# Kernel optimization log

Measured on AMD Instinct MI355X. Metric: run time of the kernel, lower is better.

The kernel has to match this reference:

```python
import jax, jax.numpy as jnp
import numpy as np

HIDDEN = 1024
N_HEADS = 16
N_KV = 4
HEAD_DIM = HIDDEN // N_HEADS  # 64


def setup_inputs() -> dict:
    key = jax.random.key(0)
    ks = jax.random.split(key, 10)
    B, S, D = 2, 2048, HIDDEN
    s = 0.02
    return {
        "hidden_states": jax.random.normal(ks[0], (B, S, D), jnp.float32),
        "attention_mask": jnp.ones((B, S), jnp.float32),
        "Wq": jax.random.normal(ks[1], (D, N_HEADS * HEAD_DIM), jnp.float32) * s,
        "bq": jnp.zeros((N_HEADS * HEAD_DIM,), jnp.float32),
        "Wk": jax.random.normal(ks[2], (D, N_KV * HEAD_DIM), jnp.float32) * s,
        "bk": jnp.zeros((N_KV * HEAD_DIM,), jnp.float32),
        "Wv": jax.random.normal(ks[3], (D, N_KV * HEAD_DIM), jnp.float32) * s,
        "bv": jnp.zeros((N_KV * HEAD_DIM,), jnp.float32),
        "Wo": jax.random.normal(ks[4], (D, D), jnp.float32) * s,
        "bo": jnp.zeros((D,), jnp.float32),
    }


def _rope(x):
    # x: [B, H, S, Dh]; half-split RoPE as in the torch module
    S, Dh = x.shape[-2], x.shape[-1]
    inv_freq = 1.0 / (10000.0 ** (jnp.arange(0, Dh, 2, dtype=jnp.float32) / Dh))
    freqs = jnp.arange(S, dtype=jnp.float32)[:, None] * inv_freq[None, :]  # [S, Dh/2]
    cos, sin = jnp.cos(freqs), jnp.sin(freqs)
    x1, x2 = jnp.split(x, 2, axis=-1)
    return jnp.concatenate([x1 * cos - x2 * sin, x1 * sin + x2 * cos], axis=-1)


def reference(hidden_states, attention_mask, Wq, bq, Wk, bk, Wv, bv, Wo, bo):
    B, S, D = hidden_states.shape
    q = (hidden_states @ Wq + bq).reshape(B, S, N_HEADS, HEAD_DIM).transpose(0, 2, 1, 3)
    k = (hidden_states @ Wk + bk).reshape(B, S, N_KV, HEAD_DIM).transpose(0, 2, 1, 3)
    v = (hidden_states @ Wv + bv).reshape(B, S, N_KV, HEAD_DIM).transpose(0, 2, 1, 3)
    q = _rope(q)
    k = _rope(k)
    rep = N_HEADS // N_KV
    k = jnp.repeat(k, rep, axis=1)  # [B, H, S, Dh]
    v = jnp.repeat(v, rep, axis=1)
    bias = (1.0 - attention_mask[:, None, None, :]) * -1e9  # [B,1,1,S]
    scores = jnp.einsum("bhqd,bhkd->bhqk", q, k) / jnp.sqrt(jnp.float32(HEAD_DIM))
    attn = jax.nn.softmax(scores + bias, axis=-1)
    out = jnp.einsum("bhqk,bhkd->bhqd", attn, v)
    out = out.transpose(0, 2, 1, 3).reshape(B, S, D)
    return out @ Wo + bo
```

## Files before the change

kernel.cpp:

```cpp
#include <hip/hip_runtime.h>

typedef __bf16 bf16;
typedef __attribute__((ext_vector_type(8))) __bf16 bf16x8;
typedef __attribute__((ext_vector_type(4))) __bf16 bf16x4;
typedef __attribute__((ext_vector_type(4))) float f32x4;

#define LOG2E 1.44269504088896340736f
#define QSCALE 0.18033688011112042f

__device__ inline void tr_tile(const float* __restrict__ in, bf16* __restrict__ out,
                               int R, int C, int bx, int by, int tid) {
    __shared__ float t[32][33];
    int tx = tid & 31, ty = tid >> 5;
    int rbase = by * 32, cbase = bx * 32;
#pragma unroll
    for (int i = 0; i < 4; i++) {
        int r = ty + i * 8;
        t[r][tx] = in[(size_t)(rbase + r) * C + cbase + tx];
    }
    __syncthreads();
#pragma unroll
    for (int i = 0; i < 4; i++) {
        int r = ty + i * 8;
        out[(size_t)(cbase + r) * R + rbase + tx] = (bf16)t[tx][r];
    }
}

__global__ __launch_bounds__(256) void prep_k(const float* __restrict__ X,
                                              const float* __restrict__ Wq,
                                              const float* __restrict__ Wk,
                                              const float* __restrict__ Wv,
                                              const float* __restrict__ Wo,
                                              const float* __restrict__ mask,
                                              bf16* __restrict__ Xb,
                                              bf16* __restrict__ WqT,
                                              bf16* __restrict__ WkT,
                                              bf16* __restrict__ WvT,
                                              bf16* __restrict__ WoT,
                                              float2* __restrict__ rt,
                                              float* __restrict__ Mb,
                                              int* __restrict__ mflags) {
    int blk = blockIdx.x, tid = threadIdx.x;
    if (blk < 2048) {
        int idx = (blk * 256 + tid) * 8;
        float4 a = *(const float4*)(X + idx);
        float4 b = *(const float4*)(X + idx + 4);
        bf16 v[8] = {(bf16)a.x, (bf16)a.y, (bf16)a.z, (bf16)a.w,
                     (bf16)b.x, (bf16)b.y, (bf16)b.z, (bf16)b.w};
        *(uint4*)(Xb + idx) = *(const uint4*)v;
    } else if (blk < 3072) {
        int t = blk - 2048; tr_tile(Wq, WqT, 1024, 1024, t & 31, t >> 5, tid);
    } else if (blk < 3328) {
        int t = blk - 3072; tr_tile(Wk, WkT, 1024, 256, t & 7, t >> 3, tid);
    } else if (blk < 3584) {
        int t = blk - 3328; tr_tile(Wv, WvT, 1024, 256, t & 7, t >> 3, tid);
    } else if (blk < 4608) {
        int t = blk - 3584; tr_tile(Wo, WoT, 1024, 1024, t & 31, t >> 5, tid);
    } else if (blk < 4864) {
        int idx = (blk - 4608) * 256 + tid;
        int s = idx >> 5, i = idx & 31;
        float inv = exp2f(-0.41524100370589830f * (float)i);
        float ang = (float)s * inv;
        rt[idx] = make_float2(cosf(ang), sinf(ang));
    } else {
        __shared__ int sflag;
        int b = blk - 4864;
        if (tid == 0) sflag = 1;
        __syncthreads();
        const float* mrow = mask + (size_t)b * 2048;
        int i0 = tid * 8;
        bool ones = true;
#pragma unroll
        for (int j = 0; j < 8; j++) {
            float m = mrow[i0 + j];
            if (m != 1.0f) ones = false;
            Mb[(size_t)b * 2048 + i0 + j] = (1.0f - m) * (-1e9f) * LOG2E;
        }
        if (!ones) sflag = 0;
        __syncthreads();
        if (tid == 0) mflags[b] = sflag;
    }
}

__global__ __launch_bounds__(256) void vtrans_k(const unsigned short* __restrict__ in,
                                                unsigned short* __restrict__ out) {
    __shared__ unsigned short t[32][33];
    int z = blockIdx.z;
    const unsigned short* ip = in + (size_t)z * 2048 * 64;
    unsigned short* op = out + (size_t)z * 2048 * 64;
    int tx = threadIdx.x & 31, ty = threadIdx.x >> 5;
    int rbase = blockIdx.y * 32, cbase = blockIdx.x * 32;
#pragma unroll
    for (int i = 0; i < 4; i++) {
        int r = ty + i * 8;
        t[r][tx] = ip[(size_t)(rbase + r) * 64 + cbase + tx];
    }
    __syncthreads();
#pragma unroll
    for (int i = 0; i < 4; i++) {
        int r = ty + i * 8;
        op[(size_t)(cbase + r) * 2048 + rbase + tx] = t[tx][r];
    }
}

__device__ __forceinline__ void gemm_main_12864(const bf16* __restrict__ A,
                                                const bf16* __restrict__ BT,
                                                int m0, int n0, int tid,
                                                f32x4 (&acc)[2][4]) {
    __shared__ bf16 As[128 * 64];
    __shared__ bf16 Bs[64 * 64];
    int w = tid >> 6, lane = tid & 63, l15 = lane & 15, quad = lane >> 4;

    int srow = lane >> 3;
    int kx = ((lane & 7) ^ srow) * 8;
    const bf16* ga0 = A + (size_t)(m0 + w * 32 + srow) * 1024 + kx;
    const bf16* gb0 = BT + (size_t)(n0 + w * 16 + srow) * 1024 + kx;
    bf16* la0 = As + (w * 32) * 64 + lane * 8;
    bf16* lb0 = Bs + (w * 16) * 64 + lane * 8;

    for (int k0 = 0; k0 < 1024; k0 += 64) {
#pragma unroll
        for (int p = 0; p < 4; p++)
            __builtin_amdgcn_global_load_lds(
                (const __attribute__((address_space(1))) unsigned int*)(ga0 + (size_t)p * 8 * 1024 + k0),
                (__attribute__((address_space(3))) unsigned int*)(la0 + p * 512), 16, 0, 0);
#pragma unroll
        for (int p = 0; p < 2; p++)
            __builtin_amdgcn_global_load_lds(
                (const __attribute__((address_space(1))) unsigned int*)(gb0 + (size_t)p * 8 * 1024 + k0),
                (__attribute__((address_space(3))) unsigned int*)(lb0 + p * 512), 16, 0, 0);
        __syncthreads();
#pragma unroll
        for (int half = 0; half < 2; half++) {
            bf16x8 a[2], bfr[4];
            int kp = ((half * 4 + quad) ^ (l15 & 7)) * 8;
#pragma unroll
            for (int i = 0; i < 2; i++)
                a[i] = *(const bf16x8*)&As[(w * 32 + i * 16 + l15) * 64 + kp];
#pragma unroll
            for (int j = 0; j < 4; j++)
                bfr[j] = *(const bf16x8*)&Bs[(j * 16 + l15) * 64 + kp];
#pragma unroll
            for (int i = 0; i < 2; i++)
#pragma unroll
                for (int j = 0; j < 4; j++)
                    acc[i][j] = __builtin_amdgcn_mfma_f32_16x16x32_bf16(a[i], bfr[j], acc[i][j], 0, 0, 0);
        }
        __syncthreads();
    }
}

__global__ __launch_bounds__(256) void qkv_gemm2(const bf16* __restrict__ Xb,
                                                 const bf16* __restrict__ WTall,
                                                 const float* __restrict__ bq,
                                                 const float* __restrict__ bk,
                                                 const float* __restrict__ bv,
                                                 const float2* __restrict__ rt,
                                                 bf16* __restrict__ Qb,
                                                 bf16* __restrict__ Kb,
                                                 bf16* __restrict__ Vb) {
    int tt = blockIdx.x, gy = blockIdx.y, tid = threadIdx.x;
    f32x4 acc[2][4] = {};
    gemm_main_12864(Xb, WTall, tt * 128, gy * 64, tid, acc);

    int w = tid >> 6, lane = tid & 63, l15 = lane & 15, quad = lane >> 4;
    const float* bias;
    bf16* dst;
    int mode, head;
    if (gy < 16)      { head = gy;      bias = bq + head * 64; dst = Qb; mode = 0; }
    else if (gy < 20) { head = gy - 16; bias = bk + head * 64; dst = Kb; mode = 1; }
    else              { head = gy - 20; bias = bv + head * 64; dst = Vb; mode = 2; }

#pragma unroll
    for (int i = 0; i < 2; i++) {
#pragma unroll
        for (int r = 0; r < 4; r++) {
            int token = tt * 128 + w * 32 + i * 16 + quad * 4 + r;
            int b = token >> 11, s = token & 2047;
            float vals[4];
#pragma unroll
            for (int j = 0; j < 4; j++) vals[j] = acc[i][j][r] + bias[j * 16 + l15];
            if (mode <= 1) {
#pragma unroll
                for (int c = 0; c < 2; c++) {
                    float2 cs2 = rt[s * 32 + c * 16 + l15];
                    float x1 = vals[c], x2 = vals[c + 2];
                    vals[c]     = x1 * cs2.x - x2 * cs2.y;
                    vals[c + 2] = x1 * cs2.y + x2 * cs2.x;
                }
            }
            if (mode == 0) {
#pragma unroll
                for (int j = 0; j < 4; j++) vals[j] *= QSCALE;
            }
            size_t base;
            if (mode == 0) base = (((size_t)b * 16 + head) * 2048 + s) * 64;
            else           base = (((size_t)b * 4  + head) * 2048 + s) * 64;
#pragma unroll
            for (int j = 0; j < 4; j++) dst[base + j * 16 + l15] = (bf16)vals[j];
        }
    }
}

__global__ __launch_bounds__(256) void oproj_gemm2(const bf16* __restrict__ Ab,
                                                   const bf16* __restrict__ WoT,
                                                   const float* __restrict__ bo,
                                                   float* __restrict__ out) {
    int tt = blockIdx.x, nt = blockIdx.y, tid = threadIdx.x;
    f32x4 acc[2][4] = {};
    gemm_main_12864(Ab, WoT, tt * 128, nt * 64, tid, acc);

    int w = tid >> 6, lane = tid & 63, l15 = lane & 15, quad = lane >> 4;
#pragma unroll
    for (int i = 0; i < 2; i++) {
#pragma unroll
        for (int r = 0; r < 4; r++) {
            int token = tt * 128 + w * 32 + i * 16 + quad * 4 + r;
#pragma unroll
            for (int j = 0; j < 4; j++) {
                int n = nt * 64 + j * 16 + l15;
                out[(size_t)token * 1024 + n] = acc[i][j][r] + bo[n];
            }
        }
    }
}

__global__ __launch_bounds__(256) void attn_k(const bf16* __restrict__ Qb,
                                              const bf16* __restrict__ Kb,
                                              const bf16* __restrict__ VbT,
                                              const float* __restrict__ Mb,
                                              const int* __restrict__ mflags,
                                              bf16* __restrict__ Ob) {
    int qt = blockIdx.x, h = blockIdx.y, b = blockIdx.z;
    int kvh = h >> 2;

    __shared__ bf16 Ks[2][64 * 64];
    __shared__ bf16 Vs[2][64 * 64];
    __shared__ unsigned short Ps[4][32 * 72];

    int tid = threadIdx.x, w = tid >> 6, lane = tid & 63, l15 = lane & 15, quad = lane >> 4;

    const bool maskOnes = (mflags[b] != 0);

    bf16x8 qa[2][2];
#pragma unroll
    for (int g = 0; g < 2; g++) {
        size_t qbase = (((size_t)b * 16 + h) * 2048 + (size_t)qt * 128 + w * 32 + g * 16 + l15) * 64;
        qa[g][0] = *(const bf16x8*)(Qb + qbase + quad * 8);
        qa[g][1] = *(const bf16x8*)(Qb + qbase + 32 + quad * 8);
    }

    f32x4 oacc[2][4] = {};
    float lsum[2] = {0.f, 0.f};

    size_t kRow = ((size_t)b * 4 + kvh) * 2048;
    size_t vRow = ((size_t)b * 4 + kvh) * 64;
    const float* mrow = Mb + (size_t)b * 2048 + quad * 4;

    int srow = (lane >> 3);
    int kx = ((lane & 7) ^ srow) * 8;
    const bf16* gk0 = Kb + (kRow + w * 16 + srow) * 64 + kx;
    const bf16* gv0 = VbT + (vRow + w * 16 + srow) * 2048 + kx;
    int lofs = (w * 16) * 64 + lane * 8;

#define STAGE(KT, BUF)                                                                              \
    do {                                                                                            \
        _Pragma("unroll")                                                                           \
        for (int p = 0; p < 2; p++) {                                                               \
            __builtin_amdgcn_global_load_lds(                                                       \
                (const __attribute__((address_space(1))) unsigned int*)(gk0 + ((size_t)(KT) * 64 + p * 8) * 64), \
                (__attribute__((address_space(3))) unsigned int*)(&Ks[BUF][0] + lofs + p * 512), 16, 0, 0); \
            __builtin_amdgcn_global_load_lds(                                                       \
                (const __attribute__((address_space(1))) unsigned int*)(gv0 + (size_t)p * 8 * 2048 + (KT) * 64), \
                (__attribute__((address_space(3))) unsigned int*)(&Vs[BUF][0] + lofs + p * 512), 16, 0, 0); \
        }                                                                                           \
    } while (0)

    STAGE(0, 0);
    __syncthreads();

    for (int kt = 0; kt < 32; kt++) {
        int cb = kt & 1;
        if (kt < 31) STAGE(kt + 1, cb ^ 1);

        const bf16* ksb = &Ks[cb][0];
        const bf16* vsb = &Vs[cb][0];

        bf16x8 ka[4][2];
#pragma unroll
        for (int c = 0; c < 4; c++) {
            int row = c * 16 + l15;
#pragma unroll
            for (int half = 0; half < 2; half++) {
                int kp = ((half * 4 + quad) ^ (l15 & 7)) * 8;
                ka[c][half] = *(const bf16x8*)&ksb[row * 64 + kp];
            }
        }

        f32x4 sc[2][4];
#pragma unroll
        for (int g = 0; g < 2; g++)
#pragma unroll
            for (int c = 0; c < 4; c++) {
                f32x4 z = {};
                z = __builtin_amdgcn_mfma_f32_16x16x32_bf16(ka[c][0], qa[g][0], z, 0, 0, 0);
                z = __builtin_amdgcn_mfma_f32_16x16x32_bf16(ka[c][1], qa[g][1], z, 0, 0, 0);
                sc[g][c] = z;
            }
        if (!maskOnes) {
#pragma unroll
            for (int c = 0; c < 4; c++) {
                f32x4 bias4 = *(const f32x4*)(mrow + kt * 64 + c * 16);
#pragma unroll
                for (int r = 0; r < 4; r++) { sc[0][c][r] += bias4[r]; sc[1][c][r] += bias4[r]; }
            }
        }

#pragma unroll
        for (int g = 0; g < 2; g++) {
            float rs = 0.f;
#pragma unroll
            for (int c = 0; c < 4; c++)
#pragma unroll
                for (int r = 0; r < 4; r++) { sc[g][c][r] = exp2f(sc[g][c][r]); rs += sc[g][c][r]; }
            lsum[g] += rs;
#pragma unroll
            for (int c = 0; c < 4; c++) {
                bf16x4 pv = {(bf16)sc[g][c][0], (bf16)sc[g][c][1], (bf16)sc[g][c][2], (bf16)sc[g][c][3]};
                *(bf16x4*)&Ps[w][(g * 16 + l15) * 72 + c * 16 + quad * 4] = pv;
            }
        }

        bf16x8 vb[4][2];
#pragma unroll
        for (int c = 0; c < 4; c++) {
            int row = c * 16 + l15;
#pragma unroll
            for (int half = 0; half < 2; half++) {
                int kp = ((half * 4 + quad) ^ (l15 & 7)) * 8;
                vb[c][half] = *(const bf16x8*)&vsb[row * 64 + kp];
            }
        }
        bf16x8 pa[2][2];
#pragma unroll
        for (int g = 0; g < 2; g++) {
            pa[g][0] = *(const bf16x8*)&Ps[w][(g * 16 + l15) * 72 + quad * 8];
            pa[g][1] = *(const bf16x8*)&Ps[w][(g * 16 + l15) * 72 + 32 + quad * 8];
        }
#pragma unroll
        for (int g = 0; g < 2; g++)
#pragma unroll
            for (int c = 0; c < 4; c++) {
                oacc[g][c] = __builtin_amdgcn_mfma_f32_16x16x32_bf16(pa[g][0], vb[c][0], oacc[g][c], 0, 0, 0);
                oacc[g][c] = __builtin_amdgcn_mfma_f32_16x16x32_bf16(pa[g][1], vb[c][1], oacc[g][c], 0, 0, 0);
            }
        __syncthreads();
    }
#undef STAGE

#pragma unroll
    for (int g = 0; g < 2; g++) {
        lsum[g] += __shfl_xor(lsum[g], 16, 64);
        lsum[g] += __shfl_xor(lsum[g], 32, 64);
        float linv[4];
#pragma unroll
        for (int r = 0; r < 4; r++) linv[r] = 1.0f / __shfl(lsum[g], quad * 4 + r, 64);
#pragma unroll
        for (int r = 0; r < 4; r++) {
            int q = qt * 128 + w * 32 + g * 16 + quad * 4 + r;
            size_t base = ((size_t)b * 2048 + q) * 1024 + h * 64;
#pragma unroll
            for (int c = 0; c < 4; c++) Ob[base + c * 16 + l15] = (bf16)(oacc[g][c][r] * linv[r]);
        }
    }
}

extern "C" void kernel_launch(void* const* d_in, const int* in_sizes, int n_in,
                              void* d_out, int out_size, void* d_ws, size_t ws_size,
                              hipStream_t stream) {
    const float* X    = (const float*)d_in[0];
    const float* mask = (const float*)d_in[1];
    const float* Wq   = (const float*)d_in[2];
    const float* bq   = (const float*)d_in[3];
    const float* Wk   = (const float*)d_in[4];
    const float* bk   = (const float*)d_in[5];
    const float* Wv   = (const float*)d_in[6];
    const float* bv   = (const float*)d_in[7];
    const float* Wo   = (const float*)d_in[8];
    const float* bo   = (const float*)d_in[9];
    float* out = (float*)d_out;
    bf16* ws  = (bf16*)d_ws;

    bf16* Xb  = ws;
    bf16* WqT = Xb + (size_t)4096 * 1024;
    bf16* WkT = WqT + 1024 * 1024;
    bf16* WvT = WkT + 256 * 1024;
    bf16* WoT = WvT + 256 * 1024;
    bf16* Qb  = WoT + 1024 * 1024;
    bf16* Kb  = Qb + (size_t)2 * 16 * 2048 * 64;
    bf16* Vb  = Kb + (size_t)2 * 4 * 2048 * 64;
    bf16* Ab  = Vb + (size_t)2 * 4 * 2048 * 64;
    float2* rt = (float2*)(Ab + (size_t)2 * 2048 * 1024);
    float* Mb  = (float*)(rt + 2048 * 32);
    int* mflags = (int*)(Mb + 2 * 2048);
    bf16* VbT = Xb;

    prep_k<<<4866, 256, 0, stream>>>(X, Wq, Wk, Wv, Wo, mask, Xb, WqT, WkT, WvT, WoT, rt, Mb, mflags);
    qkv_gemm2<<<dim3(32, 24), 256, 0, stream>>>(Xb, WqT, bq, bk, bv, rt, Qb, Kb, Vb);
    vtrans_k<<<dim3(2, 64, 8), 256, 0, stream>>>((const unsigned short*)Vb, (unsigned short*)VbT);
    attn_k<<<dim3(16, 16, 2), 256, 0, stream>>>(Qb, Kb, VbT, Mb, mflags, Ab);
    oproj_gemm2<<<dim3(32, 16), 256, 0, stream>>>(Ab, WoT, bo, out);
}
```

Before: 196.5 us.

## Write V transposed from QKV GEMM and feed P from registers into MFMA

The QKV GEMM epilogue now writes V directly in transposed [d][s] layout, so the separate vtrans kernel launch and its extra global round trip go away. In the attention kernel, the softmax probabilities stay in registers as bf16x4 fragments and feed 16x16x16 MFMAs directly, removing the per-wave shared-memory P buffer and its store/load traffic. The costs are strided 2-byte global stores for V in the GEMM epilogue, and twice as many smaller MFMA instructions in the PV product.

```diff
diff --git a/kernel.cpp b/kernel.cpp
--- a/kernel.cpp
+++ b/kernel.cpp
@@ -4,9 +4,21 @@
 typedef __attribute__((ext_vector_type(8))) __bf16 bf16x8;
 typedef __attribute__((ext_vector_type(4))) __bf16 bf16x4;
 typedef __attribute__((ext_vector_type(4))) float f32x4;
+typedef __attribute__((ext_vector_type(4))) short short4v;
 
 #define LOG2E 1.44269504088896340736f
 #define QSCALE 0.18033688011112042f
+
+static __device__ __forceinline__ f32x4 mfma16x16x16bf16(bf16x4 a, bf16x4 b, f32x4 c) {
+#if __has_builtin(__builtin_amdgcn_mfma_f32_16x16x16_bf16)
+    return __builtin_amdgcn_mfma_f32_16x16x16_bf16(a, b, c, 0, 0, 0);
+#else
+    short4v as, bs;
+    __builtin_memcpy(&as, &a, 8);
+    __builtin_memcpy(&bs, &b, 8);
+    return __builtin_amdgcn_mfma_f32_16x16x16bf16_1k(as, bs, c, 0, 0, 0);
+#endif
+}
 
 __device__ inline void tr_tile(const float* __restrict__ in, bf16* __restrict__ out,
                                int R, int C, int bx, int by, int tid) {
@@ -82,27 +94,6 @@
     }
 }
 
-__global__ __launch_bounds__(256) void vtrans_k(const unsigned short* __restrict__ in,
-                                                unsigned short* __restrict__ out) {
-    __shared__ unsigned short t[32][33];
-    int z = blockIdx.z;
-    const unsigned short* ip = in + (size_t)z * 2048 * 64;
-    unsigned short* op = out + (size_t)z * 2048 * 64;
-    int tx = threadIdx.x & 31, ty = threadIdx.x >> 5;
-    int rbase = blockIdx.y * 32, cbase = blockIdx.x * 32;
-#pragma unroll
-    for (int i = 0; i < 4; i++) {
-        int r = ty + i * 8;
-        t[r][tx] = ip[(size_t)(rbase + r) * 64 + cbase + tx];
-    }
-    __syncthreads();
-#pragma unroll
-    for (int i = 0; i < 4; i++) {
-        int r = ty + i * 8;
-        op[(size_t)(cbase + r) * 2048 + rbase + tx] = t[tx][r];
-    }
-}
-
 __device__ __forceinline__ void gemm_main_12864(const bf16* __restrict__ A,
                                                 const bf16* __restrict__ BT,
                                                 int m0, int n0, int tid,
@@ -158,18 +149,17 @@
                                                  const float2* __restrict__ rt,
                                                  bf16* __restrict__ Qb,
                                                  bf16* __restrict__ Kb,
-                                                 bf16* __restrict__ Vb) {
+                                                 bf16* __restrict__ VbT) {
     int tt = blockIdx.x, gy = blockIdx.y, tid = threadIdx.x;
     f32x4 acc[2][4] = {};
     gemm_main_12864(Xb, WTall, tt * 128, gy * 64, tid, acc);
 
     int w = tid >> 6, lane = tid & 63, l15 = lane & 15, quad = lane >> 4;
     const float* bias;
-    bf16* dst;
     int mode, head;
-    if (gy < 16)      { head = gy;      bias = bq + head * 64; dst = Qb; mode = 0; }
-    else if (gy < 20) { head = gy - 16; bias = bk + head * 64; dst = Kb; mode = 1; }
-    else              { head = gy - 20; bias = bv + head * 64; dst = Vb; mode = 2; }
+    if (gy < 16)      { head = gy;      bias = bq + head * 64; mode = 0; }
+    else if (gy < 20) { head = gy - 16; bias = bk + head * 64; mode = 1; }
+    else              { head = gy - 20; bias = bv + head * 64; mode = 2; }
 
 #pragma unroll
     for (int i = 0; i < 2; i++) {
@@ -192,12 +182,18 @@
             if (mode == 0) {
 #pragma unroll
                 for (int j = 0; j < 4; j++) vals[j] *= QSCALE;
-            }
-            size_t base;
-            if (mode == 0) base = (((size_t)b * 16 + head) * 2048 + s) * 64;
-            else           base = (((size_t)b * 4  + head) * 2048 + s) * 64;
-#pragma unroll
-            for (int j = 0; j < 4; j++) dst[base + j * 16 + l15] = (bf16)vals[j];
+                size_t base = (((size_t)b * 16 + head) * 2048 + s) * 64;
+#pragma unroll
+                for (int j = 0; j < 4; j++) Qb[base + j * 16 + l15] = (bf16)vals[j];
+            } else if (mode == 1) {
+                size_t base = (((size_t)b * 4 + head) * 2048 + s) * 64;
+#pragma unroll
+                for (int j = 0; j < 4; j++) Kb[base + j * 16 + l15] = (bf16)vals[j];
+            } else {
+                size_t vbase = ((size_t)b * 4 + head) * 64 * 2048 + s;
+#pragma unroll
+                for (int j = 0; j < 4; j++) VbT[vbase + (size_t)(j * 16 + l15) * 2048] = (bf16)vals[j];
+            }
         }
     }
 }
@@ -236,7 +232,6 @@
 
     __shared__ bf16 Ks[2][64 * 64];
     __shared__ bf16 Vs[2][64 * 64];
-    __shared__ unsigned short Ps[4][32 * 72];
 
     int tid = threadIdx.x, w = tid >> 6, lane = tid & 63, l15 = lane & 15, quad = lane >> 4;
 
@@ -316,44 +311,33 @@
             }
         }
 
+        bf16x4 pv[2][4];
 #pragma unroll
         for (int g = 0; g < 2; g++) {
             float rs = 0.f;
 #pragma unroll
-            for (int c = 0; c < 4; c++)
+            for (int c = 0; c < 4; c++) {
 #pragma unroll
                 for (int r = 0; r < 4; r++) { sc[g][c][r] = exp2f(sc[g][c][r]); rs += sc[g][c][r]; }
+                bf16x4 t = {(bf16)sc[g][c][0], (bf16)sc[g][c][1], (bf16)sc[g][c][2], (bf16)sc[g][c][3]};
+                pv[g][c] = t;
+            }
             lsum[g] += rs;
+        }
+
+#pragma unroll
+        for (int dt = 0; dt < 4; dt++) {
+            int vrow = (dt * 16 + l15) * 64;
+            int x7 = l15 & 7;
 #pragma unroll
             for (int c = 0; c < 4; c++) {
-                bf16x4 pv = {(bf16)sc[g][c][0], (bf16)sc[g][c][1], (bf16)sc[g][c][2], (bf16)sc[g][c][3]};
-                *(bf16x4*)&Ps[w][(g * 16 + l15) * 72 + c * 16 + quad * 4] = pv;
-            }
-        }
-
-        bf16x8 vb[4][2];
-#pragma unroll
-        for (int c = 0; c < 4; c++) {
-            int row = c * 16 + l15;
-#pragma unroll
-            for (int half = 0; half < 2; half++) {
-                int kp = ((half * 4 + quad) ^ (l15 & 7)) * 8;
-                vb[c][half] = *(const bf16x8*)&vsb[row * 64 + kp];
-            }
-        }
-        bf16x8 pa[2][2];
-#pragma unroll
-        for (int g = 0; g < 2; g++) {
-            pa[g][0] = *(const bf16x8*)&Ps[w][(g * 16 + l15) * 72 + quad * 8];
-            pa[g][1] = *(const bf16x8*)&Ps[w][(g * 16 + l15) * 72 + 32 + quad * 8];
-        }
-#pragma unroll
-        for (int g = 0; g < 2; g++)
-#pragma unroll
-            for (int c = 0; c < 4; c++) {
-                oacc[g][c] = __builtin_amdgcn_mfma_f32_16x16x32_bf16(pa[g][0], vb[c][0], oacc[g][c], 0, 0, 0);
-                oacc[g][c] = __builtin_amdgcn_mfma_f32_16x16x32_bf16(pa[g][1], vb[c][1], oacc[g][c], 0, 0, 0);
-            }
+                int ch = ((c * 2 + (quad >> 1)) ^ x7) * 8 + (quad & 1) * 4;
+                bf16x4 vb = *(const bf16x4*)&vsb[vrow + ch];
+#pragma unroll
+                for (int g = 0; g < 2; g++)
+                    oacc[g][dt] = mfma16x16x16bf16(pv[g][c], vb, oacc[g][dt]);
+            }
+        }
         __syncthreads();
     }
 #undef STAGE
@@ -370,7 +354,7 @@
             int q = qt * 128 + w * 32 + g * 16 + quad * 4 + r;
             size_t base = ((size_t)b * 2048 + q) * 1024 + h * 64;
 #pragma unroll
-            for (int c = 0; c < 4; c++) Ob[base + c * 16 + l15] = (bf16)(oacc[g][c][r] * linv[r]);
+            for (int dt = 0; dt < 4; dt++) Ob[base + dt * 16 + l15] = (bf16)(oacc[g][dt][r] * linv[r]);
         }
     }
 }
@@ -398,16 +382,14 @@
     bf16* WoT = WvT + 256 * 1024;
     bf16* Qb  = WoT + 1024 * 1024;
     bf16* Kb  = Qb + (size_t)2 * 16 * 2048 * 64;
-    bf16* Vb  = Kb + (size_t)2 * 4 * 2048 * 64;
-    bf16* Ab  = Vb + (size_t)2 * 4 * 2048 * 64;
+    bf16* VbT = Kb + (size_t)2 * 4 * 2048 * 64;
+    bf16* Ab  = VbT + (size_t)2 * 4 * 2048 * 64;
     float2* rt = (float2*)(Ab + (size_t)2 * 2048 * 1024);
     float* Mb  = (float*)(rt + 2048 * 32);
     int* mflags = (int*)(Mb + 2 * 2048);
-    bf16* VbT = Xb;
 
     prep_k<<<4866, 256, 0, stream>>>(X, Wq, Wk, Wv, Wo, mask, Xb, WqT, WkT, WvT, WoT, rt, Mb, mflags);
-    qkv_gemm2<<<dim3(32, 24), 256, 0, stream>>>(Xb, WqT, bq, bk, bv, rt, Qb, Kb, Vb);
-    vtrans_k<<<dim3(2, 64, 8), 256, 0, stream>>>((const unsigned short*)Vb, (unsigned short*)VbT);
+    qkv_gemm2<<<dim3(32, 24), 256, 0, stream>>>(Xb, WqT, bq, bk, bv, rt, Qb, Kb, VbT);
     attn_k<<<dim3(16, 16, 2), 256, 0, stream>>>(Qb, Kb, VbT, Mb, mflags, Ab);
     oproj_gemm2<<<dim3(32, 16), 256, 0, stream>>>(Ab, WoT, bo, out);
 }
```

Result: slower. 200.5 us (+2.0%).
